# Kernel optimization log

Hardware: AMD Instinct MI355X
Metric: run time of the kernel (lower is better)

The kernel has to match this reference:

```python
import jax, jax.numpy as jnp
import numpy as np

H = 2048          # hidden_size
E = 16            # n_routed_experts
K = 4             # num_experts_per_tok
I = 1408          # moe_intermediate_size
SH_I = 2 * I      # shared experts intermediate (n_shared_experts * moe_intermediate_size)
B, S = 1, 1024


def setup_inputs() -> dict:
    key = jax.random.key(0)
    ks = jax.random.split(key, 9)
    sc_h = 1.0 / np.sqrt(H)
    sc_i = 1.0 / np.sqrt(I)
    return {
        "hidden_states": jax.random.normal(ks[0], (B, S, H), dtype=jnp.float32),
        "w_gate": jax.random.normal(ks[1], (E, H), dtype=jnp.float32) * sc_h,
        "wg": jax.random.normal(ks[2], (E, H, I), dtype=jnp.float32) * sc_h,  # gate_proj per expert
        "wu": jax.random.normal(ks[3], (E, H, I), dtype=jnp.float32) * sc_h,  # up_proj per expert
        "wd": jax.random.normal(ks[4], (E, I, H), dtype=jnp.float32) * sc_i,  # down_proj per expert
        "sg": jax.random.normal(ks[5], (H, SH_I), dtype=jnp.float32) * sc_h,  # shared gate_proj
        "su": jax.random.normal(ks[6], (H, SH_I), dtype=jnp.float32) * sc_h,  # shared up_proj
        "sd": jax.random.normal(ks[7], (SH_I, H), dtype=jnp.float32) * (1.0 / np.sqrt(SH_I)),
    }


def reference(hidden_states, w_gate, wg, wu, wd, sg, su, sd):
    b, s, h = hidden_states.shape
    x = hidden_states.reshape(-1, h)                      # [T, H]
    T = x.shape[0]

    # --- router: softmax (fp32) -> topk -> scatter-add weights into [T, E] ---
    logits = x @ w_gate.T                                 # [T, E]
    probs = jax.nn.softmax(logits.astype(jnp.float32), axis=-1)
    top_w, top_i = jax.lax.top_k(probs, K)                # [T, K]
    routing_weight = jnp.zeros((T, E), dtype=probs.dtype)
    routing_weight = routing_weight.at[jnp.arange(T)[:, None], top_i].add(top_w)  # scatter_add_

    # --- routed experts (grouped SwiGLU MLPs), weighted combine ---
    g = jnp.einsum('th,ehi->tei', x, wg)                  # [T, E, I]
    u = jnp.einsum('th,ehi->tei', x, wu)
    act = jax.nn.silu(g) * u                              # [T, E, I]
    routed = jnp.einsum('te,tei,eih->th', routing_weight, act, wd)  # [T, H]

    # --- shared experts (always on) ---
    shared = (jax.nn.silu(x @ sg) * (x @ su)) @ sd        # [T, H]

    out = (routed + shared).astype(hidden_states.dtype)
    return out.reshape(b, s, h)
```

## Files before the change

### kernel.cpp

```cpp
#include <hip/hip_runtime.h>
#include <hip/hip_bf16.h>
#include <stdint.h>

#define T_NUM 1024
#define H_DIM 2048
#define E_NUM 16
#define TOPK 4
#define I_DIM 1408
#define SHI_DIM 2816

typedef __attribute__((ext_vector_type(4))) float f32x4;
typedef __attribute__((ext_vector_type(8))) short bf16x8;
typedef __attribute__((ext_vector_type(4))) short s16x4;

static __device__ __forceinline__ short f2bf(float f) {
    __hip_bfloat16 h = __float2bfloat16(f);
    return __builtin_bit_cast(short, h);
}
static __device__ __forceinline__ float bf2f(short s) {
    return __bfloat162float(__builtin_bit_cast(__hip_bfloat16, s));
}

static __device__ __forceinline__ void gllA16(const short* g, const short* l) {
    __builtin_amdgcn_global_load_lds(
        (const __attribute__((address_space(1))) void*)g,
        (__attribute__((address_space(3))) void*)l, 16, 0, 0);
}
static __device__ __forceinline__ void gllB16(const float* g, const float* l) {
    __builtin_amdgcn_global_load_lds(
        (const __attribute__((address_space(1))) void*)g,
        (__attribute__((address_space(3))) void*)l, 16, 0, 0);
}

__global__ void router_kernel(const float* __restrict__ x, const float* __restrict__ wgate,
                              int* __restrict__ top_e, float* __restrict__ top_w,
                              short* __restrict__ xb) {
    const int t = blockIdx.x;
    const int tid = threadIdx.x;
    __shared__ float xsh[H_DIM];
    const float* xr = x + (size_t)t * H_DIM;
    for (int h = tid; h < H_DIM; h += 256) xsh[h] = xr[h];
    __syncthreads();

    {
        short v[8];
        #pragma unroll
        for (int i = 0; i < 8; ++i) v[i] = f2bf(xsh[tid * 8 + i]);
        *reinterpret_cast<bf16x8*>(xb + (size_t)t * H_DIM + tid * 8) = *(bf16x8*)v;
    }

    const int e = tid >> 4;
    const int j = tid & 15;
    const float* wr = wgate + (size_t)e * H_DIM;
    float acc = 0.f;
    for (int h = j; h < H_DIM; h += 16) acc += xsh[h] * wr[h];
    #pragma unroll
    for (int m = 8; m >= 1; m >>= 1) acc += __shfl_down(acc, m, 16);

    __shared__ float logits[E_NUM];
    if (j == 0) logits[e] = acc;
    __syncthreads();

    if (tid == 0) {
        float mx = logits[0];
        #pragma unroll
        for (int i = 1; i < E_NUM; ++i) mx = fmaxf(mx, logits[i]);
        float p[E_NUM]; float s = 0.f;
        #pragma unroll
        for (int i = 0; i < E_NUM; ++i) { p[i] = expf(logits[i] - mx); s += p[i]; }
        const float inv = 1.f / s;
        #pragma unroll
        for (int i = 0; i < E_NUM; ++i) p[i] *= inv;
        for (int k = 0; k < TOPK; ++k) {
            float best = -1.f; int bi = 0;
            #pragma unroll
            for (int i = 0; i < E_NUM; ++i) if (p[i] > best) { best = p[i]; bi = i; }
            top_e[t * TOPK + k] = bi;
            top_w[t * TOPK + k] = best;
            p[bi] = -2.f;
        }
    }
}

__global__ void perm_kernel(const int* __restrict__ top_e,
                            int* __restrict__ offs, int* __restrict__ perm) {
    __shared__ int cnt[256][E_NUM];
    __shared__ int base[E_NUM];
    const int tid = threadIdx.x;
    int c[E_NUM];
    #pragma unroll
    for (int i = 0; i < E_NUM; ++i) c[i] = 0;
    for (int s = tid * 16; s < tid * 16 + 16; ++s) c[top_e[s]]++;
    #pragma unroll
    for (int i = 0; i < E_NUM; ++i) cnt[tid][i] = c[i];
    __syncthreads();
    if (tid < E_NUM) {
        int run = 0;
        for (int b = 0; b < 256; ++b) { int v = cnt[b][tid]; cnt[b][tid] = run; run += v; }
        base[tid] = run;
    }
    __syncthreads();
    if (tid == 0) {
        int run = 0;
        for (int e2 = 0; e2 < E_NUM; ++e2) { int v = base[e2]; base[e2] = run; offs[e2] = run; run += v; }
        offs[E_NUM] = run;
    }
    __syncthreads();
    int run[E_NUM];
    #pragma unroll
    for (int i = 0; i < E_NUM; ++i) run[i] = base[i] + cnt[tid][i];
    for (int s = tid * 16; s < tid * 16 + 16; ++s) {
        int e2 = top_e[s];
        perm[run[e2]++] = s;
    }
}

__global__ void swiglu_kernel(const short* __restrict__ g, const short* __restrict__ u,
                              short* __restrict__ act, int n8) {
    const int i = blockIdx.x * 256 + threadIdx.x;
    if (i >= n8) return;
    bf16x8 gv = *reinterpret_cast<const bf16x8*>(g + (size_t)i * 8);
    bf16x8 uv = *reinterpret_cast<const bf16x8*>(u + (size_t)i * 8);
    short o[8];
    #pragma unroll
    for (int j = 0; j < 8; ++j) {
        float gf = bf2f(gv[j]);
        float uf = bf2f(uv[j]);
        o[j] = f2bf(gf / (1.f + __expf(-gf)) * uf);
    }
    *reinterpret_cast<bf16x8*>(act + (size_t)i * 8) = *(bf16x8*)o;
}

__global__ void combine_kernel(const short* __restrict__ dr, float* __restrict__ out) {
    const int i = blockIdx.x * 256 + threadIdx.x;
    const int t = i >> 8;
    const int h8 = (i & 255) * 8;
    float s[8];
    f32x4 o0 = *reinterpret_cast<const f32x4*>(out + (size_t)t * H_DIM + h8);
    f32x4 o1 = *reinterpret_cast<const f32x4*>(out + (size_t)t * H_DIM + h8 + 4);
    #pragma unroll
    for (int j = 0; j < 4; ++j) { s[j] = o0[j]; s[4 + j] = o1[j]; }
    #pragma unroll
    for (int k = 0; k < TOPK; ++k) {
        bf16x8 v = *reinterpret_cast<const bf16x8*>(dr + ((size_t)(t * TOPK + k)) * H_DIM + h8);
        #pragma unroll
        for (int j = 0; j < 8; ++j) s[j] += bf2f(v[j]);
    }
    f32x4 r0 = { s[0], s[1], s[2], s[3] };
    f32x4 r1 = { s[4], s[5], s[6], s[7] };
    *reinterpret_cast<f32x4*>(out + (size_t)t * H_DIM + h8) = r0;
    *reinterpret_cast<f32x4*>(out + (size_t)t * H_DIM + h8 + 4) = r1;
}

template<int MODE>
__global__ __launch_bounds__(256, 3) void gemm_ring(
    const short* __restrict__ A, int lda, int Kdim,
    const float* __restrict__ B1g, const float* __restrict__ B2g, int ldb,
    void* __restrict__ Out1v, void* __restrict__ Out2v, int ldo,
    const int* __restrict__ perm, const int* __restrict__ offs,
    const float* __restrict__ top_w, int nmt, int nnt, int nsplit)
{
    __shared__ __align__(16) short As[3][128 * 32];
    __shared__ __align__(16) float Bsf[3][32 * 64];
    __shared__ int   rows_a[128];
    __shared__ int   rows_o[128];
    __shared__ float w_m[128];

    const int tid = threadIdx.x;

    int wgid = blockIdx.x;
    {
        const int nwg = gridDim.x;
        const int qq = nwg >> 3, rr = nwg & 7;
        const int xcd = wgid & 7, lin = wgid >> 3;
        wgid = (xcd < rr ? xcd * (qq + 1) : rr * (qq + 1) + (xcd - rr) * qq) + lin;
    }
    const int mt  = wgid % nmt;
    const int ntt = (wgid / nmt) % nnt;
    const int e   = wgid / (nmt * nnt);

    int off = 0, cnt = T_NUM;
    const float* B1 = B1g;
    const float* B2 = B2g;
    if constexpr (MODE == 0) {
        off = offs[e]; cnt = offs[e + 1] - off;
        if (mt * 128 >= cnt) return;
        B1 = B1g + (size_t)e * H_DIM * I_DIM;
        B2 = B2g + (size_t)e * H_DIM * I_DIM;
    }
    if constexpr (MODE == 2) {
        off = offs[e]; cnt = offs[e + 1] - off;
        if (mt * 128 >= cnt) return;
        B1 = B1g + (size_t)e * I_DIM * H_DIM;
    }
    const float* Bsel = (ntt < nsplit) ? B1 : B2;
    const int ncol = (ntt % nsplit) * 64;

    if (tid < 128) {
        const int gm = mt * 128 + tid;
        if constexpr (MODE == 0) {
            int s = perm[off + (gm < cnt ? gm : cnt - 1)];
            rows_a[tid] = s >> 2; rows_o[tid] = s; w_m[tid] = 1.f;
        } else if constexpr (MODE == 2) {
            int s = perm[off + (gm < cnt ? gm : cnt - 1)];
            rows_a[tid] = s; rows_o[tid] = s; w_m[tid] = top_w[s];
        } else {
            rows_a[tid] = gm; rows_o[tid] = gm; w_m[tid] = 1.f;
        }
    }
    __syncthreads();

    int raReg[2];
    #pragma unroll
    for (int it = 0; it < 2; ++it) raReg[it] = rows_a[it * 64 + (tid >> 2)];

    const int bk0 = tid >> 4,          const_bn0 = 0;
    const int bn4a = (tid & 15) * 4;
    const int bk1 = (tid + 256) >> 4;
    const int bn4b = ((tid + 256) & 15) * 4;

    auto stage = [&](int slot, int kt) {
        const int k0 = kt * 32;
        #pragma unroll
        for (int it = 0; it < 2; ++it) {
            const int q = it * 256 + tid;
            const int m = q >> 2;
            const int c = ((q & 3) ^ ((m >> 1) & 3)) * 8;
            gllA16(A + (size_t)raReg[it] * lda + k0 + c, &As[slot][q * 8]);
        }
        gllB16(Bsel + (size_t)(k0 + bk0) * ldb + ncol + bn4a, &Bsf[slot][bk0 * 64 + bn4a]);
        gllB16(Bsel + (size_t)(k0 + bk1) * ldb + ncol + bn4b, &Bsf[slot][bk1 * 64 + bn4b]);
    };

    f32x4 acc[4][2];
    #pragma unroll
    for (int i = 0; i < 4; ++i)
        #pragma unroll
        for (int j = 0; j < 2; ++j) acc[i][j] = (f32x4)0.f;

    const int lane = tid & 63;
    const int wr = (tid >> 7), wc = (tid >> 6) & 1;
    const int lrow = lane & 15;
    const int lko = (lane >> 4) * 8;
    const int cswz = (((lane >> 4) ^ ((lrow >> 1) & 3)) * 8);

    auto compute = [&](int slot) {
        bf16x8 af[4];
        #pragma unroll
        for (int mi = 0; mi < 4; ++mi)
            af[mi] = *reinterpret_cast<const bf16x8*>(&As[slot][(wr * 64 + mi * 16 + lrow) * 32 + cswz]);
        #pragma unroll
        for (int ni = 0; ni < 2; ++ni) {
            const int n = wc * 32 + ni * 16 + lrow;
            bf16x8 bfr;
            #pragma unroll
            for (int kk = 0; kk < 8; ++kk)
                bfr[kk] = f2bf(Bsf[slot][(lko + kk) * 64 + n]);
            #pragma unroll
            for (int mi = 0; mi < 4; ++mi)
                acc[mi][ni] = __builtin_amdgcn_mfma_f32_16x16x32_bf16(af[mi], bfr, acc[mi][ni], 0, 0, 0);
        }
    };

    const int NK = Kdim / 32;

    stage(0, 0);
    stage(1, 1);
    for (int t = 0; t < NK; ++t) {
        if (t + 1 < NK) {
            asm volatile("s_waitcnt vmcnt(4)" ::: "memory");
        } else {
            asm volatile("s_waitcnt vmcnt(0)" ::: "memory");
        }
        __builtin_amdgcn_sched_barrier(0);
        __builtin_amdgcn_s_barrier();
        compute(t % 3);
        if (t + 2 < NK) stage((t + 2) % 3, t + 2);
    }

    #pragma unroll
    for (int mi = 0; mi < 4; ++mi) {
        #pragma unroll
        for (int j = 0; j < 4; ++j) {
            const int ml = wr * 64 + mi * 16 + (lane >> 4) * 4 + j;
            const int gm = mt * 128 + ml;
            if constexpr (MODE == 0 || MODE == 2) { if (gm >= cnt) continue; }
            const int orow = (MODE == 0 || MODE == 2) ? rows_o[ml] : gm;
            const float wsc = w_m[ml];
            #pragma unroll
            for (int ni = 0; ni < 2; ++ni) {
                const int n = ncol + wc * 32 + ni * 16 + (lane & 15);
                const float v = acc[mi][ni][j];
                if constexpr (MODE == 0 || MODE == 1) {
                    short* o = (short*)((ntt < nsplit) ? Out1v : Out2v);
                    o[(size_t)orow * ldo + n] = f2bf(v);
                } else if constexpr (MODE == 2) {
                    ((short*)Out1v)[(size_t)orow * ldo + n] = f2bf(v * wsc);
                } else {
                    ((float*)Out1v)[(size_t)orow * ldo + n] = v;
                }
            }
        }
    }
}

extern "C" void kernel_launch(void* const* d_in, const int* in_sizes, int n_in,
                              void* d_out, int out_size, void* d_ws, size_t ws_size,
                              hipStream_t stream) {
    const float* x     = (const float*)d_in[0];
    const float* wgate = (const float*)d_in[1];
    const float* wg    = (const float*)d_in[2];
    const float* wu    = (const float*)d_in[3];
    const float* wd    = (const float*)d_in[4];
    const float* sg    = (const float*)d_in[5];
    const float* su    = (const float*)d_in[6];
    const float* sd    = (const float*)d_in[7];
    float* out = (float*)d_out;

    uintptr_t p = (uintptr_t)d_ws;
    auto alloc = [&](size_t bytes) {
        p = (p + 255) & ~(uintptr_t)255;
        void* r = (void*)p; p += bytes; return r;
    };
    int*   top_e = (int*)alloc((size_t)T_NUM * TOPK * sizeof(int));
    float* top_w = (float*)alloc((size_t)T_NUM * TOPK * sizeof(float));
    int*   offs  = (int*)alloc((E_NUM + 1) * sizeof(int));
    int*   perm  = (int*)alloc((size_t)T_NUM * TOPK * sizeof(int));
    short* xb    = (short*)alloc((size_t)T_NUM * H_DIM * 2);
    short* g_r   = (short*)alloc((size_t)T_NUM * TOPK * I_DIM * 2);
    short* u_r   = (short*)alloc((size_t)T_NUM * TOPK * I_DIM * 2);
    short* act_r = (short*)alloc((size_t)T_NUM * TOPK * I_DIM * 2);
    short* g_s   = (short*)alloc((size_t)T_NUM * SHI_DIM * 2);
    short* u_s   = (short*)alloc((size_t)T_NUM * SHI_DIM * 2);
    short* act_s = (short*)alloc((size_t)T_NUM * SHI_DIM * 2);
    short* dr    = (short*)alloc((size_t)T_NUM * TOPK * H_DIM * 2);

    router_kernel<<<T_NUM, 256, 0, stream>>>(x, wgate, top_e, top_w, xb);
    perm_kernel<<<1, 256, 0, stream>>>(top_e, offs, perm);

    const int nmtT = T_NUM / 128;
    const int nnI  = I_DIM / 64;
    const int nnH  = H_DIM / 64;
    const int nnS  = SHI_DIM / 64;

    gemm_ring<1><<<nmtT * (2 * nnS), 256, 0, stream>>>(
        xb, H_DIM, H_DIM, sg, su, SHI_DIM, g_s, u_s, SHI_DIM,
        nullptr, nullptr, nullptr, nmtT, 2 * nnS, nnS);
    swiglu_kernel<<<(T_NUM * SHI_DIM / 8 + 255) / 256, 256, 0, stream>>>(
        g_s, u_s, act_s, T_NUM * SHI_DIM / 8);
    gemm_ring<3><<<nmtT * nnH, 256, 0, stream>>>(
        act_s, SHI_DIM, SHI_DIM, sd, nullptr, H_DIM, out, nullptr, H_DIM,
        nullptr, nullptr, nullptr, nmtT, nnH, nnH);

    gemm_ring<0><<<nmtT * (2 * nnI) * E_NUM, 256, 0, stream>>>(
        xb, H_DIM, H_DIM, wg, wu, I_DIM, g_r, u_r, I_DIM,
        perm, offs, nullptr, nmtT, 2 * nnI, nnI);
    swiglu_kernel<<<(T_NUM * TOPK * I_DIM / 8 + 255) / 256, 256, 0, stream>>>(
        g_r, u_r, act_r, T_NUM * TOPK * I_DIM / 8);
    gemm_ring<2><<<nmtT * nnH * E_NUM, 256, 0, stream>>>(
        act_r, I_DIM, I_DIM, wd, nullptr, H_DIM, dr, nullptr, H_DIM,
        perm, offs, top_w, nmtT, nnH, nnH);
    combine_kernel<<<T_NUM * H_DIM / 8 / 256, 256, 0, stream>>>(dr, out);
}
```

Before: 593.9 us.

## Pre-transpose weights to bf16 and use 128x128 bf16 GEMM tiles

Adds a tiled transpose-and-convert kernel that turns every fp32 weight matrix into a K-contiguous bf16 copy in workspace on each call. The GEMMs then load B with swizzled 16-byte global-to-LDS copies, the same way as A, instead of reading scalar fp32 values from LDS and converting them inside the MFMA loop. The output tile grows from 128x64 to 128x128, the pipeline drops from three LDS buffers to two, and the fused gate/up launches become separate launches. The trade-off is an extra full pass over all weights each call (fp32 read plus bf16 write), in exchange for cheaper inner loops and more compute per LDS load.

```diff
diff --git a/kernel.cpp b/kernel.cpp
--- a/kernel.cpp
+++ b/kernel.cpp
@@ -21,12 +21,7 @@
     return __bfloat162float(__builtin_bit_cast(__hip_bfloat16, s));
 }
 
-static __device__ __forceinline__ void gllA16(const short* g, const short* l) {
-    __builtin_amdgcn_global_load_lds(
-        (const __attribute__((address_space(1))) void*)g,
-        (__attribute__((address_space(3))) void*)l, 16, 0, 0);
-}
-static __device__ __forceinline__ void gllB16(const float* g, const float* l) {
+static __device__ __forceinline__ void gll16(const short* g, const short* l) {
     __builtin_amdgcn_global_load_lds(
         (const __attribute__((address_space(1))) void*)g,
         (__attribute__((address_space(3))) void*)l, 16, 0, 0);
@@ -115,6 +110,33 @@
     }
 }
 
+__global__ void tconv_kernel(const float* __restrict__ src, short* __restrict__ dst,
+                             int R, int C) {
+    __shared__ float t[64][65];
+    const int c0 = blockIdx.x * 64, r0 = blockIdx.y * 64;
+    const size_t mo = (size_t)blockIdx.z * R * C;
+    const float* s = src + mo;
+    short* d = dst + mo;
+    const int tid = threadIdx.x;
+    #pragma unroll
+    for (int it = 0; it < 4; ++it) {
+        const int q = it * 256 + tid;
+        const int r = q >> 4, c4 = (q & 15) * 4;
+        f32x4 v = *reinterpret_cast<const f32x4*>(s + (size_t)(r0 + r) * C + c0 + c4);
+        t[r][c4] = v[0]; t[r][c4 + 1] = v[1]; t[r][c4 + 2] = v[2]; t[r][c4 + 3] = v[3];
+    }
+    __syncthreads();
+    #pragma unroll
+    for (int it = 0; it < 2; ++it) {
+        const int q = it * 256 + tid;
+        const int c = q >> 3, r8 = (q & 7) * 8;
+        short v[8];
+        #pragma unroll
+        for (int i = 0; i < 8; ++i) v[i] = f2bf(t[r8 + i][c]);
+        *reinterpret_cast<bf16x8*>(d + (size_t)(c0 + c) * R + r0 + r8) = *(bf16x8*)v;
+    }
+}
+
 __global__ void swiglu_kernel(const short* __restrict__ g, const short* __restrict__ u,
                               short* __restrict__ act, int n8) {
     const int i = blockIdx.x * 256 + threadIdx.x;
@@ -153,48 +175,40 @@
 }
 
 template<int MODE>
-__global__ __launch_bounds__(256, 3) void gemm_ring(
+__global__ __launch_bounds__(256, 3) void gemm_bf(
     const short* __restrict__ A, int lda, int Kdim,
-    const float* __restrict__ B1g, const float* __restrict__ B2g, int ldb,
-    void* __restrict__ Out1v, void* __restrict__ Out2v, int ldo,
+    const short* __restrict__ Bg,
+    void* __restrict__ Outv, int ldo,
     const int* __restrict__ perm, const int* __restrict__ offs,
-    const float* __restrict__ top_w, int nmt, int nnt, int nsplit)
+    const float* __restrict__ top_w, int nmt, int nnt)
 {
-    __shared__ __align__(16) short As[3][128 * 32];
-    __shared__ __align__(16) float Bsf[3][32 * 64];
+    constexpr int BK = 32;
+    __shared__ __align__(16) short As[2][128 * 32];
+    __shared__ __align__(16) short Bs[2][128 * 32];
     __shared__ int   rows_a[128];
     __shared__ int   rows_o[128];
     __shared__ float w_m[128];
 
     const int tid = threadIdx.x;
 
-    int wgid = blockIdx.x;
+    int wg = blockIdx.x;
     {
         const int nwg = gridDim.x;
         const int qq = nwg >> 3, rr = nwg & 7;
-        const int xcd = wgid & 7, lin = wgid >> 3;
-        wgid = (xcd < rr ? xcd * (qq + 1) : rr * (qq + 1) + (xcd - rr) * qq) + lin;
-    }
-    const int mt  = wgid % nmt;
-    const int ntt = (wgid / nmt) % nnt;
-    const int e   = wgid / (nmt * nnt);
+        const int xcd = wg & 7, lin = wg >> 3;
+        wg = (xcd < rr ? xcd * (qq + 1) : rr * (qq + 1) + (xcd - rr) * qq) + lin;
+    }
+    const int mt = wg % nmt;
+    const int nt = (wg / nmt) % nnt;
+    const int e  = wg / (nmt * nnt);
 
     int off = 0, cnt = T_NUM;
-    const float* B1 = B1g;
-    const float* B2 = B2g;
-    if constexpr (MODE == 0) {
+    const short* Bt = Bg;
+    if constexpr (MODE == 0 || MODE == 2) {
         off = offs[e]; cnt = offs[e + 1] - off;
         if (mt * 128 >= cnt) return;
-        B1 = B1g + (size_t)e * H_DIM * I_DIM;
-        B2 = B2g + (size_t)e * H_DIM * I_DIM;
-    }
-    if constexpr (MODE == 2) {
-        off = offs[e]; cnt = offs[e + 1] - off;
-        if (mt * 128 >= cnt) return;
-        B1 = B1g + (size_t)e * I_DIM * H_DIM;
-    }
-    const float* Bsel = (ntt < nsplit) ? B1 : B2;
-    const int ncol = (ntt % nsplit) * 64;
+        Bt = Bg + (size_t)e * ((size_t)nnt * 128) * Kdim;
+    }
 
     if (tid < 128) {
         const int gm = mt * 128 + tid;
@@ -214,68 +228,63 @@
     #pragma unroll
     for (int it = 0; it < 2; ++it) raReg[it] = rows_a[it * 64 + (tid >> 2)];
 
-    const int bk0 = tid >> 4,          const_bn0 = 0;
-    const int bn4a = (tid & 15) * 4;
-    const int bk1 = (tid + 256) >> 4;
-    const int bn4b = ((tid + 256) & 15) * 4;
-
-    auto stage = [&](int slot, int kt) {
-        const int k0 = kt * 32;
+    auto stage = [&](int buf, int kt) {
+        const int k0 = kt * BK;
         #pragma unroll
         for (int it = 0; it < 2; ++it) {
             const int q = it * 256 + tid;
             const int m = q >> 2;
             const int c = ((q & 3) ^ ((m >> 1) & 3)) * 8;
-            gllA16(A + (size_t)raReg[it] * lda + k0 + c, &As[slot][q * 8]);
-        }
-        gllB16(Bsel + (size_t)(k0 + bk0) * ldb + ncol + bn4a, &Bsf[slot][bk0 * 64 + bn4a]);
-        gllB16(Bsel + (size_t)(k0 + bk1) * ldb + ncol + bn4b, &Bsf[slot][bk1 * 64 + bn4b]);
+            gll16(A + (size_t)raReg[it] * lda + k0 + c, &As[buf][q * 8]);
+        }
+        #pragma unroll
+        for (int it = 0; it < 2; ++it) {
+            const int q = it * 256 + tid;
+            const int n = q >> 2;
+            const int c = ((q & 3) ^ ((n >> 1) & 3)) * 8;
+            gll16(Bt + (size_t)(nt * 128 + n) * Kdim + k0 + c, &Bs[buf][q * 8]);
+        }
     };
 
-    f32x4 acc[4][2];
+    f32x4 acc[4][4];
     #pragma unroll
     for (int i = 0; i < 4; ++i)
         #pragma unroll
-        for (int j = 0; j < 2; ++j) acc[i][j] = (f32x4)0.f;
+        for (int j = 0; j < 4; ++j) acc[i][j] = (f32x4)0.f;
 
     const int lane = tid & 63;
     const int wr = (tid >> 7), wc = (tid >> 6) & 1;
     const int lrow = lane & 15;
-    const int lko = (lane >> 4) * 8;
     const int cswz = (((lane >> 4) ^ ((lrow >> 1) & 3)) * 8);
 
-    auto compute = [&](int slot) {
+    auto compute = [&](int buf) {
         bf16x8 af[4];
         #pragma unroll
         for (int mi = 0; mi < 4; ++mi)
-            af[mi] = *reinterpret_cast<const bf16x8*>(&As[slot][(wr * 64 + mi * 16 + lrow) * 32 + cswz]);
-        #pragma unroll
-        for (int ni = 0; ni < 2; ++ni) {
-            const int n = wc * 32 + ni * 16 + lrow;
-            bf16x8 bfr;
-            #pragma unroll
-            for (int kk = 0; kk < 8; ++kk)
-                bfr[kk] = f2bf(Bsf[slot][(lko + kk) * 64 + n]);
+            af[mi] = *reinterpret_cast<const bf16x8*>(&As[buf][(wr * 64 + mi * 16 + lrow) * 32 + cswz]);
+        #pragma unroll
+        for (int ni = 0; ni < 4; ++ni) {
+            bf16x8 bfr = *reinterpret_cast<const bf16x8*>(&Bs[buf][(wc * 64 + ni * 16 + lrow) * 32 + cswz]);
             #pragma unroll
             for (int mi = 0; mi < 4; ++mi)
                 acc[mi][ni] = __builtin_amdgcn_mfma_f32_16x16x32_bf16(af[mi], bfr, acc[mi][ni], 0, 0, 0);
         }
     };
 
-    const int NK = Kdim / 32;
-
+    const int NK = Kdim / BK;
     stage(0, 0);
-    stage(1, 1);
-    for (int t = 0; t < NK; ++t) {
-        if (t + 1 < NK) {
+    int buf = 0;
+    for (int kt = 0; kt < NK; ++kt) {
+        if (kt + 1 < NK) {
+            stage(buf ^ 1, kt + 1);
             asm volatile("s_waitcnt vmcnt(4)" ::: "memory");
         } else {
             asm volatile("s_waitcnt vmcnt(0)" ::: "memory");
         }
-        __builtin_amdgcn_sched_barrier(0);
         __builtin_amdgcn_s_barrier();
-        compute(t % 3);
-        if (t + 2 < NK) stage((t + 2) % 3, t + 2);
+        compute(buf);
+        __builtin_amdgcn_s_barrier();
+        buf ^= 1;
     }
 
     #pragma unroll
@@ -288,16 +297,15 @@
             const int orow = (MODE == 0 || MODE == 2) ? rows_o[ml] : gm;
             const float wsc = w_m[ml];
             #pragma unroll
-            for (int ni = 0; ni < 2; ++ni) {
-                const int n = ncol + wc * 32 + ni * 16 + (lane & 15);
+            for (int ni = 0; ni < 4; ++ni) {
+                const int n = nt * 128 + wc * 64 + ni * 16 + (lane & 15);
                 const float v = acc[mi][ni][j];
                 if constexpr (MODE == 0 || MODE == 1) {
-                    short* o = (short*)((ntt < nsplit) ? Out1v : Out2v);
-                    o[(size_t)orow * ldo + n] = f2bf(v);
+                    ((short*)Outv)[(size_t)orow * ldo + n] = f2bf(v);
                 } else if constexpr (MODE == 2) {
-                    ((short*)Out1v)[(size_t)orow * ldo + n] = f2bf(v * wsc);
+                    ((short*)Outv)[(size_t)orow * ldo + n] = f2bf(v * wsc);
                 } else {
-                    ((float*)Out1v)[(size_t)orow * ldo + n] = v;
+                    ((float*)Outv)[(size_t)orow * ldo + n] = v;
                 }
             }
         }
@@ -327,6 +335,15 @@
     int*   offs  = (int*)alloc((E_NUM + 1) * sizeof(int));
     int*   perm  = (int*)alloc((size_t)T_NUM * TOPK * sizeof(int));
     short* xb    = (short*)alloc((size_t)T_NUM * H_DIM * 2);
+
+    const size_t wguSz = (size_t)E_NUM * H_DIM * I_DIM * 2;
+    const size_t shSz  = (size_t)H_DIM * SHI_DIM * 2;
+    short* wgT = (short*)alloc(wguSz);
+    short* wuT = (short*)alloc(wguSz);
+    short* wdT = (short*)alloc(wguSz);
+    short* sgT = (short*)alloc(shSz);
+    short* suT = (short*)alloc(shSz);
+    short* sdT = (short*)alloc(shSz);
     short* g_r   = (short*)alloc((size_t)T_NUM * TOPK * I_DIM * 2);
     short* u_r   = (short*)alloc((size_t)T_NUM * TOPK * I_DIM * 2);
     short* act_r = (short*)alloc((size_t)T_NUM * TOPK * I_DIM * 2);
@@ -338,27 +355,33 @@
     router_kernel<<<T_NUM, 256, 0, stream>>>(x, wgate, top_e, top_w, xb);
     perm_kernel<<<1, 256, 0, stream>>>(top_e, offs, perm);
 
+    tconv_kernel<<<dim3(I_DIM / 64, H_DIM / 64, E_NUM), 256, 0, stream>>>(wg, wgT, H_DIM, I_DIM);
+    tconv_kernel<<<dim3(I_DIM / 64, H_DIM / 64, E_NUM), 256, 0, stream>>>(wu, wuT, H_DIM, I_DIM);
+    tconv_kernel<<<dim3(H_DIM / 64, I_DIM / 64, E_NUM), 256, 0, stream>>>(wd, wdT, I_DIM, H_DIM);
+    tconv_kernel<<<dim3(SHI_DIM / 64, H_DIM / 64, 1), 256, 0, stream>>>(sg, sgT, H_DIM, SHI_DIM);
+    tconv_kernel<<<dim3(SHI_DIM / 64, H_DIM / 64, 1), 256, 0, stream>>>(su, suT, H_DIM, SHI_DIM);
+    tconv_kernel<<<dim3(H_DIM / 64, SHI_DIM / 64, 1), 256, 0, stream>>>(sd, sdT, SHI_DIM, H_DIM);
+
     const int nmtT = T_NUM / 128;
-    const int nnI  = I_DIM / 64;
-    const int nnH  = H_DIM / 64;
-    const int nnS  = SHI_DIM / 64;
-
-    gemm_ring<1><<<nmtT * (2 * nnS), 256, 0, stream>>>(
-        xb, H_DIM, H_DIM, sg, su, SHI_DIM, g_s, u_s, SHI_DIM,
-        nullptr, nullptr, nullptr, nmtT, 2 * nnS, nnS);
+    const int nnI = I_DIM / 128;
+    const int nnH = H_DIM / 128;
+    const int nnS = SHI_DIM / 128;
+
+    gemm_bf<1><<<nmtT * nnS, 256, 0, stream>>>(xb, H_DIM, H_DIM, sgT, g_s, SHI_DIM,
+                                               nullptr, nullptr, nullptr, nmtT, nnS);
+    gemm_bf<1><<<nmtT * nnS, 256, 0, stream>>>(xb, H_DIM, H_DIM, suT, u_s, SHI_DIM,
+                                               nullptr, nullptr, nullptr, nmtT, nnS);
     swiglu_kernel<<<(T_NUM * SHI_DIM / 8 + 255) / 256, 256, 0, stream>>>(
         g_s, u_s, act_s, T_NUM * SHI_DIM / 8);
-    gemm_ring<3><<<nmtT * nnH, 256, 0, stream>>>(
-        act_s, SHI_DIM, SHI_DIM, sd, nullptr, H_DIM, out, nullptr, H_DIM,
-        nullptr, nullptr, nullptr, nmtT, nnH, nnH);
-
-    gemm_ring<0><<<nmtT * (2 * nnI) * E_NUM, 256, 0, stream>>>(
-        xb, H_DIM, H_DIM, wg, wu, I_DIM, g_r, u_r, I_DIM,
-        perm, offs, nullptr, nmtT, 2 * nnI, nnI);
+    gemm_bf<3><<<nmtT * nnH, 256, 0, stream>>>(act_s, SHI_DIM, SHI_DIM, sdT, out, H_DIM,
+                                               nullptr, nullptr, nullptr, nmtT, nnH);
+    gemm_bf<0><<<nmtT * nnI * E_NUM, 256, 0, stream>>>(xb, H_DIM, H_DIM, wgT, g_r, I_DIM,
+                                                       perm, offs, nullptr, nmtT, nnI);
+    gemm_bf<0><<<nmtT * nnI * E_NUM, 256, 0, stream>>>(xb, H_DIM, H_DIM, wuT, u_r, I_DIM,
+                                                       perm, offs, nullptr, nmtT, nnI);
     swiglu_kernel<<<(T_NUM * TOPK * I_DIM / 8 + 255) / 256, 256, 0, stream>>>(
         g_r, u_r, act_r, T_NUM * TOPK * I_DIM / 8);
-    gemm_ring<2><<<nmtT * nnH * E_NUM, 256, 0, stream>>>(
-        act_r, I_DIM, I_DIM, wd, nullptr, H_DIM, dr, nullptr, H_DIM,
-        perm, offs, top_w, nmtT, nnH, nnH);
+    gemm_bf<2><<<nmtT * nnH * E_NUM, 256, 0, stream>>>(act_r, I_DIM, I_DIM, wdT, dr, H_DIM,
+                                                       perm, offs, top_w, nmtT, nnH);
     combine_kernel<<<T_NUM * H_DIM / 8 / 256, 256, 0, stream>>>(dr, out);
 }
```

New measurement: 629.1 us. +5.9%, slower.
